# Kernel optimization log

Hardware: AMD Instinct MI355X
Metric: run time of the kernel (lower is better)

The kernel has to match this reference:

```python
import jax, jax.numpy as jnp
import numpy as np

DIM = 128
HEADS = 4


def setup_inputs() -> dict:
    key = jax.random.key(0)
    ks = jax.random.split(key, 6)
    B_, N, C = 2048, 49, DIM
    nW = 64
    x = jax.random.normal(ks[0], (B_, N, C), dtype=jnp.float32)
    mask = jax.random.normal(ks[1], (nW, N, N), dtype=jnp.float32)
    qkv_w = jax.random.normal(ks[2], (3 * C, C), dtype=jnp.float32) * 0.02
    qkv_b = jnp.zeros((3 * C,), dtype=jnp.float32)
    proj_w = jax.random.normal(ks[3], (C, C), dtype=jnp.float32) * 0.02
    proj_b = jnp.zeros((C,), dtype=jnp.float32)
    return {"x": x, "mask": mask, "qkv_w": qkv_w, "qkv_b": qkv_b,
            "proj_w": proj_w, "proj_b": proj_b}


def reference(x, mask, qkv_w, qkv_b, proj_w, proj_b):
    B_, N, C = x.shape
    H = HEADS
    Dh = C // H
    scale = Dh ** (-0.5)
    # fused QKV projection: [B_, N, 3C]
    qkv = x @ qkv_w.T + qkv_b
    qkv = qkv.reshape(B_, N, 3, H, Dh).transpose(2, 0, 3, 1, 4)  # [3, B_, H, N, Dh]
    q, k, v = qkv[0] * scale, qkv[1], qkv[2]
    attn = jnp.einsum('bhqd,bhkd->bhqk', q, k)  # [B_, H, N, N]
    nW = mask.shape[0]
    # add per-window additive mask: broadcast over images and heads
    attn = attn.reshape(B_ // nW, nW, H, N, N) + mask[None, :, None, :, :]
    attn = jax.nn.softmax(attn.reshape(B_, H, N, N), axis=-1)
    out = jnp.einsum('bhqk,bhkd->bhqd', attn, v)  # [B_, H, N, Dh]
    out = out.transpose(0, 2, 1, 3).reshape(B_, N, C)
    return out @ proj_w.T + proj_b
```

## Files before the change

kernel.cpp:

```cpp
#include <hip/hip_runtime.h>

typedef __bf16 bf16_t;
typedef __bf16 bf16x2 __attribute__((ext_vector_type(2)));
typedef __bf16 bf16x4 __attribute__((ext_vector_type(4)));
typedef __bf16 bf16x8 __attribute__((ext_vector_type(8)));
typedef float  f32x4  __attribute__((ext_vector_type(4)));
typedef float  f32x4u __attribute__((ext_vector_type(4), aligned(4)));
typedef unsigned int u32;

#define MFMA16(a, b, c) __builtin_amdgcn_mfma_f32_16x16x32_bf16((a), (b), (c), 0, 0, 0)

#define ROWB 272


union W8 { u32 u[4]; bf16x8 v; };

__device__ __forceinline__ u32 pack2(float a, float b) {
    union { bf16x2 h; u32 u; } c;
    c.h[0] = (bf16_t)a; c.h[1] = (bf16_t)b;
    return c.u;
}

__device__ __forceinline__ void st4(char* base, int row, int byteoff, bf16x4 v) {
    *(bf16x4*)(base + row * ROWB + byteoff) = v;
}
__device__ __forceinline__ bf16x8 ld8(const char* base, int row, int byteoff) {
    return *(const bf16x8*)(base + row * ROWB + byteoff);
}

__device__ __forceinline__ bf16x8 redist4(u32 w0, u32 w1, u32 w2, u32 w3,
                                          bool gl, bool gh) {
    u32 wd[4] = {w0, w1, w2, w3};
    u32 X[4], Y[4], Z[4];
    #pragma unroll
    for (int j = 0; j < 4; ++j) X[j] = __shfl_xor(wd[j], 16);
    #pragma unroll
    for (int j = 0; j < 4; ++j) Y[j] = __shfl_xor(wd[j], 32);
    #pragma unroll
    for (int j = 0; j < 4; ++j) Z[j] = __shfl_xor(X[j], 32);
    W8 u;
    #pragma unroll
    for (int t = 0; t < 4; ++t) {
        int j0 = t & 1;
        int j1 = j0 + 2;
        u32 lo, hi;
        if (t < 2) { lo = gl ? Z[j0] : wd[j0]; hi = gl ? X[j1] : Y[j1]; }
        else       { lo = gl ? Y[j0] : X[j0];  hi = gl ? wd[j1] : Z[j1]; }
        u.u[t] = gh ? hi : lo;
    }
    return u.v;
}

__global__ void wconv_kernel(const float* __restrict__ qw, const float* __restrict__ pw,
                             bf16_t* __restrict__ o) {
    int i = (blockIdx.x * 256 + threadIdx.x) * 4;
    const float* src = (i < 49152) ? (qw + i) : (pw + (i - 49152));
    float4 f = *(const float4*)src;
    bf16x4 h;
    h[0] = (bf16_t)f.x; h[1] = (bf16_t)f.y; h[2] = (bf16_t)f.z; h[3] = (bf16_t)f.w;
    *(bf16x4*)(o + i) = h;
}

template<int USEB>
__device__ __forceinline__ bf16x8 ldw(const float* __restrict__ wf,
                                      const bf16_t* __restrict__ wb, int idx) {
    if constexpr (USEB) {
        return *(const bf16x8*)(wb + idx);
    } else {
        float4 f0 = *(const float4*)(wf + idx);
        float4 f1 = *(const float4*)(wf + idx + 4);
        bf16x8 r;
        r[0] = (bf16_t)f0.x; r[1] = (bf16_t)f0.y; r[2] = (bf16_t)f0.z; r[3] = (bf16_t)f0.w;
        r[4] = (bf16_t)f1.x; r[5] = (bf16_t)f1.y; r[6] = (bf16_t)f1.z; r[7] = (bf16_t)f1.w;
        return r;
    }
}

template<int USEB>
__device__ __forceinline__ void pass_rowmajor(
    const char* xs, const float* __restrict__ wf, const bf16_t* __restrict__ wb,
    int rowbase, const float* __restrict__ biasp, float scale,
    int g, int c0, bool gl, bool gh, bf16x8 out[4])
{
    f32x4 acc[2][4];
    #pragma unroll
    for (int d = 0; d < 2; ++d)
        #pragma unroll
        for (int mt = 0; mt < 4; ++mt) acc[d][mt] = {0.f, 0.f, 0.f, 0.f};
    #pragma unroll
    for (int ks = 0; ks < 4; ++ks) {
        bf16x8 w0 = ldw<USEB>(wf, wb, (rowbase + c0) * 128 + 32 * ks + 8 * g);
        bf16x8 w1 = ldw<USEB>(wf, wb, (rowbase + 16 + c0) * 128 + 32 * ks + 8 * g);
        #pragma unroll
        for (int mt = 0; mt < 4; ++mt) {
            bf16x8 xf = ld8(xs, 16 * mt + c0, (32 * ks + 8 * g) * 2);
            acc[0][mt] = MFMA16(w0, xf, acc[0][mt]);
            acc[1][mt] = MFMA16(w1, xf, acc[1][mt]);
        }
    }
    float4 b0 = *(const float4*)(biasp + rowbase + 4 * g);
    float4 b1 = *(const float4*)(biasp + rowbase + 16 + 4 * g);
    #pragma unroll
    for (int t = 0; t < 4; ++t) {
        out[t] = redist4(
            pack2((acc[0][t][0] + b0.x) * scale, (acc[0][t][1] + b0.y) * scale),
            pack2((acc[0][t][2] + b0.z) * scale, (acc[0][t][3] + b0.w) * scale),
            pack2((acc[1][t][0] + b1.x) * scale, (acc[1][t][1] + b1.y) * scale),
            pack2((acc[1][t][2] + b1.z) * scale, (acc[1][t][3] + b1.w) * scale),
            gl, gh);
    }
}

template<int USEB>
__global__ __launch_bounds__(256, 4) void winattn_kernel(
    const float* __restrict__ xg, const float* __restrict__ maskg,
    const float* __restrict__ qwg, const float* __restrict__ qbg,
    const float* __restrict__ pwg, const float* __restrict__ pbg,
    const bf16_t* __restrict__ wqb, const bf16_t* __restrict__ wpb,
    const int nW, float* __restrict__ outg)
{
    __shared__ char xs[17408];

    const int b    = blockIdx.x;
    const int tid  = threadIdx.x;
    const int w    = tid >> 6;
    const int lane = tid & 63;
    const int g    = lane >> 4;
    const int c0   = lane & 15;
    const bool gl  = (g & 1) != 0, gh = (g & 2) != 0;
    const int h    = w;

    {
        const float4* xb = (const float4*)(xg + (long)b * 6272);
        #pragma unroll
        for (int it = 0; it < 7; ++it) {
            int i = tid + it * 256;
            if (i < 1568) {
                float4 f = xb[i];
                int row = i >> 5, colb = (i & 31) << 3;
                bf16x4 hq;
                hq[0] = (bf16_t)f.x; hq[1] = (bf16_t)f.y; hq[2] = (bf16_t)f.z; hq[3] = (bf16_t)f.w;
                st4(xs, row, colb, hq);
            }
        }
        #pragma unroll
        for (int it = 0; it < 4; ++it) {
            int i = tid + it * 256;
            if (i < 960) {
                int row = 49 + (i >> 6), byteo = (i & 63) << 2;
                *(u32*)(xs + row * ROWB + byteo) = 0u;
            }
        }
    }
    __syncthreads();

    const float qs = 0.17677669529663687f;
    bf16x8 qfr[4], ka[4];
    pass_rowmajor<USEB>(xs, qwg, wqb, 32 * h,       qbg, qs,  g, c0, gl, gh, qfr);
    pass_rowmajor<USEB>(xs, qwg, wqb, 128 + 32 * h, qbg, 1.f, g, c0, gl, gh, ka);

    bf16x8 va[2][2];
    {
        const int rb = 256 + 32 * h;
        f32x4 acc[4][2];
        #pragma unroll
        for (int mt = 0; mt < 4; ++mt)
            #pragma unroll
            for (int d = 0; d < 2; ++d) acc[mt][d] = {0.f, 0.f, 0.f, 0.f};
        #pragma unroll
        for (int ks = 0; ks < 4; ++ks) {
            bf16x8 w0 = ldw<USEB>(qwg, wqb, (rb + c0) * 128 + 32 * ks + 8 * g);
            bf16x8 w1 = ldw<USEB>(qwg, wqb, (rb + 16 + c0) * 128 + 32 * ks + 8 * g);
            #pragma unroll
            for (int mt = 0; mt < 4; ++mt) {
                bf16x8 xf = ld8(xs, 16 * mt + c0, (32 * ks + 8 * g) * 2);
                acc[mt][0] = MFMA16(xf, w0, acc[mt][0]);
                acc[mt][1] = MFMA16(xf, w1, acc[mt][1]);
            }
        }
        float vb0 = qbg[rb + c0];
        float vb1 = qbg[rb + 16 + c0];
        #pragma unroll
        for (int kt = 0; kt < 2; ++kt) {
            va[0][kt] = redist4(
                pack2(acc[2 * kt][0][0] + vb0, acc[2 * kt][0][1] + vb0),
                pack2(acc[2 * kt][0][2] + vb0, acc[2 * kt][0][3] + vb0),
                pack2(acc[2 * kt + 1][0][0] + vb0, acc[2 * kt + 1][0][1] + vb0),
                pack2(acc[2 * kt + 1][0][2] + vb0, acc[2 * kt + 1][0][3] + vb0),
                gl, gh);
            va[1][kt] = redist4(
                pack2(acc[2 * kt][1][0] + vb1, acc[2 * kt][1][1] + vb1),
                pack2(acc[2 * kt][1][2] + vb1, acc[2 * kt][1][3] + vb1),
                pack2(acc[2 * kt + 1][1][0] + vb1, acc[2 * kt + 1][1][1] + vb1),
                pack2(acc[2 * kt + 1][1][2] + vb1, acc[2 * kt + 1][1][3] + vb1),
                gl, gh);
        }
    }
    __syncthreads();

    const float* mrow = maskg + (long)(b % nW) * 2401;
    #pragma unroll
    for (int nt = 0; nt < 4; ++nt) {
        f32x4 s[4];
        #pragma unroll
        for (int kt = 0; kt < 4; ++kt) s[kt] = {0.f, 0.f, 0.f, 0.f};
        #pragma unroll
        for (int kt = 0; kt < 4; ++kt)
            s[kt] = MFMA16(ka[kt], qfr[nt], s[kt]);

        {
            int q  = 16 * nt + c0;
            int qm = q < 49 ? q : 48;
            const float* mr = mrow + qm * 49;
            f32x4u m0 = *(const f32x4u*)(mr + 4 * g);
            f32x4u m1 = *(const f32x4u*)(mr + 16 + 4 * g);
            f32x4u m2 = *(const f32x4u*)(mr + 32 + 4 * g);
            float m48 = mr[48];
            #pragma unroll
            for (int r = 0; r < 4; ++r) {
                s[0][r] += m0[r]; s[1][r] += m1[r]; s[2][r] += m2[r];
            }
            s[3][0] = (g == 0) ? s[3][0] + m48 : -1e30f;
            s[3][1] = -1e30f; s[3][2] = -1e30f; s[3][3] = -1e30f;
        }

        float mx = -1e30f;
        #pragma unroll
        for (int kt = 0; kt < 4; ++kt)
            #pragma unroll
            for (int r = 0; r < 4; ++r) mx = fmaxf(mx, s[kt][r]);
        mx = fmaxf(mx, __shfl_xor(mx, 16));
        mx = fmaxf(mx, __shfl_xor(mx, 32));

        float sum = 0.f;
        u32 wd[8];
        #pragma unroll
        for (int kt = 0; kt < 4; ++kt) {
            float e0 = __expf(s[kt][0] - mx), e1 = __expf(s[kt][1] - mx);
            float e2 = __expf(s[kt][2] - mx), e3 = __expf(s[kt][3] - mx);
            sum += (e0 + e1) + (e2 + e3);
            wd[2 * kt]     = pack2(e0, e1);
            wd[2 * kt + 1] = pack2(e2, e3);
        }
        sum += __shfl_xor(sum, 16);
        sum += __shfl_xor(sum, 32);
        float inv = 1.f / sum;

        bf16x8 pa0 = redist4(wd[0], wd[1], wd[2], wd[3], gl, gh);
        bf16x8 pa1 = redist4(wd[4], wd[5], wd[6], wd[7], gl, gh);

        f32x4 oo[2];
        oo[0] = {0.f, 0.f, 0.f, 0.f}; oo[1] = {0.f, 0.f, 0.f, 0.f};
        oo[0] = MFMA16(va[0][0], pa0, oo[0]);
        oo[0] = MFMA16(va[0][1], pa1, oo[0]);
        oo[1] = MFMA16(va[1][0], pa0, oo[1]);
        oo[1] = MFMA16(va[1][1], pa1, oo[1]);

        int q = 16 * nt + c0;
        #pragma unroll
        for (int dt = 0; dt < 2; ++dt) {
            bf16x4 t;
            t[0] = (bf16_t)(oo[dt][0] * inv); t[1] = (bf16_t)(oo[dt][1] * inv);
            t[2] = (bf16_t)(oo[dt][2] * inv); t[3] = (bf16_t)(oo[dt][3] * inv);
            st4(xs, q, (32 * h + 16 * dt + 4 * g) * 2, t);
        }
    }
    __syncthreads();

    {
        f32x4 acc[2][4];
        #pragma unroll
        for (int nt = 0; nt < 2; ++nt)
            #pragma unroll
            for (int mt = 0; mt < 4; ++mt) acc[nt][mt] = {0.f, 0.f, 0.f, 0.f};
        #pragma unroll
        for (int ks = 0; ks < 4; ++ks) {
            bf16x8 p0 = ldw<USEB>(pwg, wpb, (32 * w + c0) * 128 + 32 * ks + 8 * g);
            bf16x8 p1 = ldw<USEB>(pwg, wpb, (32 * w + 16 + c0) * 128 + 32 * ks + 8 * g);
            #pragma unroll
            for (int mt = 0; mt < 4; ++mt) {
                bf16x8 af = ld8(xs, 16 * mt + c0, (32 * ks + 8 * g) * 2);
                acc[0][mt] = MFMA16(p0, af, acc[0][mt]);
                acc[1][mt] = MFMA16(p1, af, acc[1][mt]);
            }
        }
        float4 pb0 = *(const float4*)(pbg + 32 * w + 4 * g);
        float4 pb1 = *(const float4*)(pbg + 32 * w + 16 + 4 * g);
        float* ob = outg + (long)b * 6272;
        #pragma unroll
        for (int nt = 0; nt < 2; ++nt) {
            float4 pb = nt ? pb1 : pb0;
            #pragma unroll
            for (int mt = 0; mt < 4; ++mt) {
                int tok = 16 * mt + c0;
                if (tok < 49) {
                    float4 t;
                    t.x = acc[nt][mt][0] + pb.x;
                    t.y = acc[nt][mt][1] + pb.y;
                    t.z = acc[nt][mt][2] + pb.z;
                    t.w = acc[nt][mt][3] + pb.w;
                    *(float4*)(ob + tok * 128 + 32 * w + 16 * nt + 4 * g) = t;
                }
            }
        }
    }
}

extern "C" void kernel_launch(void* const* d_in, const int* in_sizes, int n_in,
                              void* d_out, int out_size, void* d_ws, size_t ws_size,
                              hipStream_t stream) {
    const float* xg  = (const float*)d_in[0];
    const float* mg  = (const float*)d_in[1];
    const float* qwg = (const float*)d_in[2];
    const float* qbg = (const float*)d_in[3];
    const float* pwg = (const float*)d_in[4];
    const float* pbg = (const float*)d_in[5];
    float* outg = (float*)d_out;

    const int B  = in_sizes[0] / (49 * 128);
    const int nW = in_sizes[1] / (49 * 49);

    int use_wbf = (d_ws != nullptr && ws_size >= 131072) ? 1 : 0;
    bf16_t* wqb = (bf16_t*)d_ws;
    bf16_t* wpb = use_wbf ? (wqb + 49152) : nullptr;

    if (use_wbf) {
        wconv_kernel<<<64, 256, 0, stream>>>(qwg, pwg, wqb);
        winattn_kernel<1><<<B, 256, 0, stream>>>(
            xg, mg, qwg, qbg, pwg, pbg, wqb, wpb, nW, outg);
    } else {
        winattn_kernel<0><<<B, 256, 0, stream>>>(
            xg, mg, qwg, qbg, pwg, pbg, nullptr, nullptr, nW, outg);
    }
}
```

Measured before the change: 67.36 us.

## Use 16x16x16 MFMA for attention to drop cross-lane shuffle redistribution

Switches the QK^T and PV products from 16x16x32 MFMA with shuffle-based fragment redistribution (redist4) to 16x16x16 MFMA, whose operand layout matches the projection accumulator layout directly. This removes many __shfl_xor ops and selects, but doubles the number of MFMA issues for attention. It also prefetches the projection weights into registers before the barrier and relaxes launch bounds from 4 to 2 blocks per CU, which may raise register use and reduce occupancy.

```diff
diff --git a/kernel.cpp b/kernel.cpp
--- a/kernel.cpp
+++ b/kernel.cpp
@@ -6,20 +6,27 @@
 typedef __bf16 bf16x8 __attribute__((ext_vector_type(8)));
 typedef float  f32x4  __attribute__((ext_vector_type(4)));
 typedef float  f32x4u __attribute__((ext_vector_type(4), aligned(4)));
+typedef short  s16x4  __attribute__((ext_vector_type(4)));
 typedef unsigned int u32;
 
-#define MFMA16(a, b, c) __builtin_amdgcn_mfma_f32_16x16x32_bf16((a), (b), (c), 0, 0, 0)
+#define MFMA32(a, b, c) __builtin_amdgcn_mfma_f32_16x16x32_bf16((a), (b), (c), 0, 0, 0)
+
+union B4u { bf16x4 h; s16x4 s; };
+__device__ __forceinline__ f32x4 MFMA16(bf16x4 a, bf16x4 b, f32x4 c) {
+#if __has_builtin(__builtin_amdgcn_mfma_f32_16x16x16_bf16)
+    return __builtin_amdgcn_mfma_f32_16x16x16_bf16(a, b, c, 0, 0, 0);
+#elif __has_builtin(__builtin_amdgcn_mfma_f32_16x16x16bf16_1k)
+    B4u ua, ub; ua.h = a; ub.h = b;
+    return __builtin_amdgcn_mfma_f32_16x16x16bf16_1k(ua.s, ub.s, c, 0, 0, 0);
+#else
+    f32x4 d = c;
+    asm volatile("v_mfma_f32_16x16x16_bf16 %0, %1, %2, %0"
+                 : "+v"(d) : "v"(a), "v"(b));
+    return d;
+#endif
+}
 
 #define ROWB 272
-
-
-union W8 { u32 u[4]; bf16x8 v; };
-
-__device__ __forceinline__ u32 pack2(float a, float b) {
-    union { bf16x2 h; u32 u; } c;
-    c.h[0] = (bf16_t)a; c.h[1] = (bf16_t)b;
-    return c.u;
-}
 
 __device__ __forceinline__ void st4(char* base, int row, int byteoff, bf16x4 v) {
     *(bf16x4*)(base + row * ROWB + byteoff) = v;
@@ -27,28 +34,27 @@
 __device__ __forceinline__ bf16x8 ld8(const char* base, int row, int byteoff) {
     return *(const bf16x8*)(base + row * ROWB + byteoff);
 }
-
-__device__ __forceinline__ bf16x8 redist4(u32 w0, u32 w1, u32 w2, u32 w3,
-                                          bool gl, bool gh) {
-    u32 wd[4] = {w0, w1, w2, w3};
-    u32 X[4], Y[4], Z[4];
-    #pragma unroll
-    for (int j = 0; j < 4; ++j) X[j] = __shfl_xor(wd[j], 16);
-    #pragma unroll
-    for (int j = 0; j < 4; ++j) Y[j] = __shfl_xor(wd[j], 32);
-    #pragma unroll
-    for (int j = 0; j < 4; ++j) Z[j] = __shfl_xor(X[j], 32);
-    W8 u;
-    #pragma unroll
-    for (int t = 0; t < 4; ++t) {
-        int j0 = t & 1;
-        int j1 = j0 + 2;
-        u32 lo, hi;
-        if (t < 2) { lo = gl ? Z[j0] : wd[j0]; hi = gl ? X[j1] : Y[j1]; }
-        else       { lo = gl ? Y[j0] : X[j0];  hi = gl ? wd[j1] : Z[j1]; }
-        u.u[t] = gh ? hi : lo;
-    }
-    return u.v;
+__device__ __forceinline__ void stx(char* buf, int i, float4 f) {
+    bf16x4 hq;
+    hq[0] = (bf16_t)f.x; hq[1] = (bf16_t)f.y; hq[2] = (bf16_t)f.z; hq[3] = (bf16_t)f.w;
+    st4(buf, i >> 5, (i & 31) << 3, hq);
+}
+
+__device__ __forceinline__ bf16x4 cvt4b(f32x4 v, float4 bias, float sc) {
+    bf16x4 t;
+    t[0] = (bf16_t)((v[0] + bias.x) * sc);
+    t[1] = (bf16_t)((v[1] + bias.y) * sc);
+    t[2] = (bf16_t)((v[2] + bias.z) * sc);
+    t[3] = (bf16_t)((v[3] + bias.w) * sc);
+    return t;
+}
+__device__ __forceinline__ bf16x4 cvt4s(f32x4 v, float bias) {
+    bf16x4 t;
+    t[0] = (bf16_t)(v[0] + bias);
+    t[1] = (bf16_t)(v[1] + bias);
+    t[2] = (bf16_t)(v[2] + bias);
+    t[3] = (bf16_t)(v[3] + bias);
+    return t;
 }
 
 __global__ void wconv_kernel(const float* __restrict__ qw, const float* __restrict__ pw,
@@ -76,43 +82,9 @@
     }
 }
 
+
 template<int USEB>
-__device__ __forceinline__ void pass_rowmajor(
-    const char* xs, const float* __restrict__ wf, const bf16_t* __restrict__ wb,
-    int rowbase, const float* __restrict__ biasp, float scale,
-    int g, int c0, bool gl, bool gh, bf16x8 out[4])
-{
-    f32x4 acc[2][4];
-    #pragma unroll
-    for (int d = 0; d < 2; ++d)
-        #pragma unroll
-        for (int mt = 0; mt < 4; ++mt) acc[d][mt] = {0.f, 0.f, 0.f, 0.f};
-    #pragma unroll
-    for (int ks = 0; ks < 4; ++ks) {
-        bf16x8 w0 = ldw<USEB>(wf, wb, (rowbase + c0) * 128 + 32 * ks + 8 * g);
-        bf16x8 w1 = ldw<USEB>(wf, wb, (rowbase + 16 + c0) * 128 + 32 * ks + 8 * g);
-        #pragma unroll
-        for (int mt = 0; mt < 4; ++mt) {
-            bf16x8 xf = ld8(xs, 16 * mt + c0, (32 * ks + 8 * g) * 2);
-            acc[0][mt] = MFMA16(w0, xf, acc[0][mt]);
-            acc[1][mt] = MFMA16(w1, xf, acc[1][mt]);
-        }
-    }
-    float4 b0 = *(const float4*)(biasp + rowbase + 4 * g);
-    float4 b1 = *(const float4*)(biasp + rowbase + 16 + 4 * g);
-    #pragma unroll
-    for (int t = 0; t < 4; ++t) {
-        out[t] = redist4(
-            pack2((acc[0][t][0] + b0.x) * scale, (acc[0][t][1] + b0.y) * scale),
-            pack2((acc[0][t][2] + b0.z) * scale, (acc[0][t][3] + b0.w) * scale),
-            pack2((acc[1][t][0] + b1.x) * scale, (acc[1][t][1] + b1.y) * scale),
-            pack2((acc[1][t][2] + b1.z) * scale, (acc[1][t][3] + b1.w) * scale),
-            gl, gh);
-    }
-}
-
-template<int USEB>
-__global__ __launch_bounds__(256, 4) void winattn_kernel(
+__global__ __launch_bounds__(256, 2) void winattn_kernel(
     const float* __restrict__ xg, const float* __restrict__ maskg,
     const float* __restrict__ qwg, const float* __restrict__ qbg,
     const float* __restrict__ pwg, const float* __restrict__ pbg,
@@ -127,7 +99,6 @@
     const int lane = tid & 63;
     const int g    = lane >> 4;
     const int c0   = lane & 15;
-    const bool gl  = (g & 1) != 0, gh = (g & 2) != 0;
     const int h    = w;
 
     {
@@ -135,13 +106,7 @@
         #pragma unroll
         for (int it = 0; it < 7; ++it) {
             int i = tid + it * 256;
-            if (i < 1568) {
-                float4 f = xb[i];
-                int row = i >> 5, colb = (i & 31) << 3;
-                bf16x4 hq;
-                hq[0] = (bf16_t)f.x; hq[1] = (bf16_t)f.y; hq[2] = (bf16_t)f.z; hq[3] = (bf16_t)f.w;
-                st4(xs, row, colb, hq);
-            }
+            if (i < 1568) { float4 f = xb[i]; stx(xs, i, f); }
         }
         #pragma unroll
         for (int it = 0; it < 4; ++it) {
@@ -155,13 +120,63 @@
     __syncthreads();
 
     const float qs = 0.17677669529663687f;
-    bf16x8 qfr[4], ka[4];
-    pass_rowmajor<USEB>(xs, qwg, wqb, 32 * h,       qbg, qs,  g, c0, gl, gh, qfr);
-    pass_rowmajor<USEB>(xs, qwg, wqb, 128 + 32 * h, qbg, 1.f, g, c0, gl, gh, ka);
-
-    bf16x8 va[2][2];
-    {
-        const int rb = 256 + 32 * h;
+
+    bf16x4 qfr[2][4];
+    {
+        f32x4 acc[2][4];
+        #pragma unroll
+        for (int d = 0; d < 2; ++d)
+            #pragma unroll
+            for (int mt = 0; mt < 4; ++mt) acc[d][mt] = {0.f, 0.f, 0.f, 0.f};
+        #pragma unroll
+        for (int ks = 0; ks < 4; ++ks) {
+            bf16x8 w0 = ldw<USEB>(qwg, wqb, (32*h + c0) * 128 + 32*ks + 8*g);
+            bf16x8 w1 = ldw<USEB>(qwg, wqb, (32*h + 16 + c0) * 128 + 32*ks + 8*g);
+            #pragma unroll
+            for (int mt = 0; mt < 4; ++mt) {
+                bf16x8 xf = ld8(xs, 16*mt + c0, (32*ks + 8*g) * 2);
+                acc[0][mt] = MFMA32(w0, xf, acc[0][mt]);
+                acc[1][mt] = MFMA32(w1, xf, acc[1][mt]);
+            }
+        }
+        float4 b0 = *(const float4*)(qbg + 32*h + 4*g);
+        float4 b1 = *(const float4*)(qbg + 32*h + 16 + 4*g);
+        #pragma unroll
+        for (int qt = 0; qt < 4; ++qt) {
+            qfr[0][qt] = cvt4b(acc[0][qt], b0, qs);
+            qfr[1][qt] = cvt4b(acc[1][qt], b1, qs);
+        }
+    }
+
+    bf16x4 kfr[4][2];
+    {
+        f32x4 acc[2][4];
+        #pragma unroll
+        for (int d = 0; d < 2; ++d)
+            #pragma unroll
+            for (int mt = 0; mt < 4; ++mt) acc[d][mt] = {0.f, 0.f, 0.f, 0.f};
+        #pragma unroll
+        for (int ks = 0; ks < 4; ++ks) {
+            bf16x8 w0 = ldw<USEB>(qwg, wqb, (128 + 32*h + c0) * 128 + 32*ks + 8*g);
+            bf16x8 w1 = ldw<USEB>(qwg, wqb, (128 + 32*h + 16 + c0) * 128 + 32*ks + 8*g);
+            #pragma unroll
+            for (int mt = 0; mt < 4; ++mt) {
+                bf16x8 xf = ld8(xs, 16*mt + c0, (32*ks + 8*g) * 2);
+                acc[0][mt] = MFMA32(w0, xf, acc[0][mt]);
+                acc[1][mt] = MFMA32(w1, xf, acc[1][mt]);
+            }
+        }
+        float4 b0 = *(const float4*)(qbg + 128 + 32*h + 4*g);
+        float4 b1 = *(const float4*)(qbg + 128 + 32*h + 16 + 4*g);
+        #pragma unroll
+        for (int kt = 0; kt < 4; ++kt) {
+            kfr[kt][0] = cvt4b(acc[0][kt], b0, 1.f);
+            kfr[kt][1] = cvt4b(acc[1][kt], b1, 1.f);
+        }
+    }
+
+    bf16x4 vfr[2][4];
+    {
         f32x4 acc[4][2];
         #pragma unroll
         for (int mt = 0; mt < 4; ++mt)
@@ -169,52 +184,44 @@
             for (int d = 0; d < 2; ++d) acc[mt][d] = {0.f, 0.f, 0.f, 0.f};
         #pragma unroll
         for (int ks = 0; ks < 4; ++ks) {
-            bf16x8 w0 = ldw<USEB>(qwg, wqb, (rb + c0) * 128 + 32 * ks + 8 * g);
-            bf16x8 w1 = ldw<USEB>(qwg, wqb, (rb + 16 + c0) * 128 + 32 * ks + 8 * g);
-            #pragma unroll
-            for (int mt = 0; mt < 4; ++mt) {
-                bf16x8 xf = ld8(xs, 16 * mt + c0, (32 * ks + 8 * g) * 2);
-                acc[mt][0] = MFMA16(xf, w0, acc[mt][0]);
-                acc[mt][1] = MFMA16(xf, w1, acc[mt][1]);
-            }
-        }
-        float vb0 = qbg[rb + c0];
-        float vb1 = qbg[rb + 16 + c0];
-        #pragma unroll
-        for (int kt = 0; kt < 2; ++kt) {
-            va[0][kt] = redist4(
-                pack2(acc[2 * kt][0][0] + vb0, acc[2 * kt][0][1] + vb0),
-                pack2(acc[2 * kt][0][2] + vb0, acc[2 * kt][0][3] + vb0),
-                pack2(acc[2 * kt + 1][0][0] + vb0, acc[2 * kt + 1][0][1] + vb0),
-                pack2(acc[2 * kt + 1][0][2] + vb0, acc[2 * kt + 1][0][3] + vb0),
-                gl, gh);
-            va[1][kt] = redist4(
-                pack2(acc[2 * kt][1][0] + vb1, acc[2 * kt][1][1] + vb1),
-                pack2(acc[2 * kt][1][2] + vb1, acc[2 * kt][1][3] + vb1),
-                pack2(acc[2 * kt + 1][1][0] + vb1, acc[2 * kt + 1][1][1] + vb1),
-                pack2(acc[2 * kt + 1][1][2] + vb1, acc[2 * kt + 1][1][3] + vb1),
-                gl, gh);
+            bf16x8 w0 = ldw<USEB>(qwg, wqb, (256 + 32*h + c0) * 128 + 32*ks + 8*g);
+            bf16x8 w1 = ldw<USEB>(qwg, wqb, (256 + 32*h + 16 + c0) * 128 + 32*ks + 8*g);
+            #pragma unroll
+            for (int mt = 0; mt < 4; ++mt) {
+                bf16x8 xf = ld8(xs, 16*mt + c0, (32*ks + 8*g) * 2);
+                acc[mt][0] = MFMA32(xf, w0, acc[mt][0]);
+                acc[mt][1] = MFMA32(xf, w1, acc[mt][1]);
+            }
+        }
+        float vb0 = qbg[256 + 32*h + c0];
+        float vb1 = qbg[256 + 32*h + 16 + c0];
+        #pragma unroll
+        for (int kt = 0; kt < 4; ++kt) {
+            vfr[0][kt] = cvt4s(acc[kt][0], vb0);
+            vfr[1][kt] = cvt4s(acc[kt][1], vb1);
         }
     }
     __syncthreads();
 
     const float* mrow = maskg + (long)(b % nW) * 2401;
     #pragma unroll
-    for (int nt = 0; nt < 4; ++nt) {
+    for (int qt = 0; qt < 4; ++qt) {
         f32x4 s[4];
         #pragma unroll
         for (int kt = 0; kt < 4; ++kt) s[kt] = {0.f, 0.f, 0.f, 0.f};
         #pragma unroll
-        for (int kt = 0; kt < 4; ++kt)
-            s[kt] = MFMA16(ka[kt], qfr[nt], s[kt]);
+        for (int kt = 0; kt < 4; ++kt) {
+            s[kt] = MFMA16(kfr[kt][0], qfr[0][qt], s[kt]);
+            s[kt] = MFMA16(kfr[kt][1], qfr[1][qt], s[kt]);
+        }
 
         {
-            int q  = 16 * nt + c0;
+            int q  = 16*qt + c0;
             int qm = q < 49 ? q : 48;
             const float* mr = mrow + qm * 49;
-            f32x4u m0 = *(const f32x4u*)(mr + 4 * g);
-            f32x4u m1 = *(const f32x4u*)(mr + 16 + 4 * g);
-            f32x4u m2 = *(const f32x4u*)(mr + 32 + 4 * g);
+            f32x4u m0 = *(const f32x4u*)(mr + 4*g);
+            f32x4u m1 = *(const f32x4u*)(mr + 16 + 4*g);
+            f32x4u m2 = *(const f32x4u*)(mr + 32 + 4*g);
             float m48 = mr[48];
             #pragma unroll
             for (int r = 0; r < 4; ++r) {
@@ -233,38 +240,46 @@
         mx = fmaxf(mx, __shfl_xor(mx, 32));
 
         float sum = 0.f;
-        u32 wd[8];
+        bf16x4 p[4];
         #pragma unroll
         for (int kt = 0; kt < 4; ++kt) {
             float e0 = __expf(s[kt][0] - mx), e1 = __expf(s[kt][1] - mx);
             float e2 = __expf(s[kt][2] - mx), e3 = __expf(s[kt][3] - mx);
             sum += (e0 + e1) + (e2 + e3);
-            wd[2 * kt]     = pack2(e0, e1);
-            wd[2 * kt + 1] = pack2(e2, e3);
+            bf16x4 pk;
+            pk[0] = (bf16_t)e0; pk[1] = (bf16_t)e1;
+            pk[2] = (bf16_t)e2; pk[3] = (bf16_t)e3;
+            p[kt] = pk;
         }
         sum += __shfl_xor(sum, 16);
         sum += __shfl_xor(sum, 32);
         float inv = 1.f / sum;
 
-        bf16x8 pa0 = redist4(wd[0], wd[1], wd[2], wd[3], gl, gh);
-        bf16x8 pa1 = redist4(wd[4], wd[5], wd[6], wd[7], gl, gh);
-
         f32x4 oo[2];
         oo[0] = {0.f, 0.f, 0.f, 0.f}; oo[1] = {0.f, 0.f, 0.f, 0.f};
-        oo[0] = MFMA16(va[0][0], pa0, oo[0]);
-        oo[0] = MFMA16(va[0][1], pa1, oo[0]);
-        oo[1] = MFMA16(va[1][0], pa0, oo[1]);
-        oo[1] = MFMA16(va[1][1], pa1, oo[1]);
-
-        int q = 16 * nt + c0;
+        #pragma unroll
+        for (int kt = 0; kt < 4; ++kt) {
+            oo[0] = MFMA16(vfr[0][kt], p[kt], oo[0]);
+            oo[1] = MFMA16(vfr[1][kt], p[kt], oo[1]);
+        }
+        int q = 16*qt + c0;
         #pragma unroll
         for (int dt = 0; dt < 2; ++dt) {
             bf16x4 t;
             t[0] = (bf16_t)(oo[dt][0] * inv); t[1] = (bf16_t)(oo[dt][1] * inv);
             t[2] = (bf16_t)(oo[dt][2] * inv); t[3] = (bf16_t)(oo[dt][3] * inv);
-            st4(xs, q, (32 * h + 16 * dt + 4 * g) * 2, t);
-        }
-    }
+            st4(xs, q, (32*h + 16*dt + 4*g) * 2, t);
+        }
+    }
+
+    bf16x8 pwf[4][2];
+    #pragma unroll
+    for (int ks = 0; ks < 4; ++ks) {
+        pwf[ks][0] = ldw<USEB>(pwg, wpb, (32*w + c0) * 128 + 32*ks + 8*g);
+        pwf[ks][1] = ldw<USEB>(pwg, wpb, (32*w + 16 + c0) * 128 + 32*ks + 8*g);
+    }
+    float4 pb0 = *(const float4*)(pbg + 32*w + 4*g);
+    float4 pb1 = *(const float4*)(pbg + 32*w + 16 + 4*g);
     __syncthreads();
 
     {
@@ -275,31 +290,27 @@
             for (int mt = 0; mt < 4; ++mt) acc[nt][mt] = {0.f, 0.f, 0.f, 0.f};
         #pragma unroll
         for (int ks = 0; ks < 4; ++ks) {
-            bf16x8 p0 = ldw<USEB>(pwg, wpb, (32 * w + c0) * 128 + 32 * ks + 8 * g);
-            bf16x8 p1 = ldw<USEB>(pwg, wpb, (32 * w + 16 + c0) * 128 + 32 * ks + 8 * g);
-            #pragma unroll
-            for (int mt = 0; mt < 4; ++mt) {
-                bf16x8 af = ld8(xs, 16 * mt + c0, (32 * ks + 8 * g) * 2);
-                acc[0][mt] = MFMA16(p0, af, acc[0][mt]);
-                acc[1][mt] = MFMA16(p1, af, acc[1][mt]);
-            }
-        }
-        float4 pb0 = *(const float4*)(pbg + 32 * w + 4 * g);
-        float4 pb1 = *(const float4*)(pbg + 32 * w + 16 + 4 * g);
+            #pragma unroll
+            for (int mt = 0; mt < 4; ++mt) {
+                bf16x8 af = ld8(xs, 16*mt + c0, (32*ks + 8*g) * 2);
+                acc[0][mt] = MFMA32(pwf[ks][0], af, acc[0][mt]);
+                acc[1][mt] = MFMA32(pwf[ks][1], af, acc[1][mt]);
+            }
+        }
         float* ob = outg + (long)b * 6272;
         #pragma unroll
         for (int nt = 0; nt < 2; ++nt) {
             float4 pb = nt ? pb1 : pb0;
             #pragma unroll
             for (int mt = 0; mt < 4; ++mt) {
-                int tok = 16 * mt + c0;
+                int tok = 16*mt + c0;
                 if (tok < 49) {
                     float4 t;
                     t.x = acc[nt][mt][0] + pb.x;
                     t.y = acc[nt][mt][1] + pb.y;
                     t.z = acc[nt][mt][2] + pb.z;
                     t.w = acc[nt][mt][3] + pb.w;
-                    *(float4*)(ob + tok * 128 + 32 * w + 16 * nt + 4 * g) = t;
+                    *(float4*)(ob + tok*128 + 32*w + 16*nt + 4*g) = t;
                 }
             }
         }
@@ -320,11 +331,9 @@
     const int B  = in_sizes[0] / (49 * 128);
     const int nW = in_sizes[1] / (49 * 49);
 
-    int use_wbf = (d_ws != nullptr && ws_size >= 131072) ? 1 : 0;
-    bf16_t* wqb = (bf16_t*)d_ws;
-    bf16_t* wpb = use_wbf ? (wqb + 49152) : nullptr;
-
-    if (use_wbf) {
+    if (d_ws != nullptr && ws_size >= 131072) {
+        bf16_t* wqb = (bf16_t*)d_ws;
+        bf16_t* wpb = wqb + 49152;
         wconv_kernel<<<64, 256, 0, stream>>>(qwg, pwg, wqb);
         winattn_kernel<1><<<B, 256, 0, stream>>>(
             xg, mg, qwg, qbg, pwg, pbg, wqb, wpb, nW, outg);
```

Result: faster. 64.92 us (-3.6%).
